# Performance work log

Hardware: AMD Instinct MI355X
Metric: run time of the kernel (lower is better)

## Reference

```python
import jax, jax.numpy as jnp
import numpy as np

H = 12           # num_heads
D_MODEL = 768
SCALE = (D_MODEL // H) ** -0.5  # qk_scale default: head_dim**-0.5


def _attn_mask(q, k, v, mask):
    # sim: (b, i, j); mask broadcast over query dim (mask.unsqueeze(1) in torch)
    sim = jnp.einsum('bid,bjd->bij', q, k) + mask[:, None, :]
    a = jax.nn.softmax(sim, axis=-1)
    return jnp.einsum('bij,bjd->bid', a, v)


def setup_inputs() -> dict:
    key = jax.random.key(0)
    k0, k1, k2, k3 = jax.random.split(key, 4)
    B, F, n, D = 16, 8, 196, 768
    N = 1 + F * n  # cls + frames*patches = 1569
    x = jax.random.normal(k0, (B, N, D), jnp.float32)
    x_mask = jax.random.normal(k1, (B, N), jnp.float32)  # additive attention mask
    Wqkv = jax.random.normal(k2, (3 * D, D), jnp.float32) * (D ** -0.5)
    Wproj = jax.random.normal(k3, (D, D), jnp.float32) * (D ** -0.5)
    bproj = jnp.zeros((D,), jnp.float32)
    return {"x": x, "x_mask": x_mask, "Wqkv": Wqkv, "Wproj": Wproj,
            "bproj": bproj, "f": F}


def reference(x, x_mask, Wqkv, Wproj, bproj, f):
    B, N, D = x.shape
    h = H
    d = D // h
    # qkv projection (qkv_bias=False), split into q,k,v
    qkv = x @ Wqkv.T                       # (B, N, 3D)
    q, k, v = jnp.split(qkv, 3, axis=-1)

    def to_heads(t):  # 'b n (h d) -> (b h) n d'
        return t.reshape(B, N, h, d).transpose(0, 2, 1, 3).reshape(B * h, N, d)

    q, k, v = map(to_heads, (q, k, v))
    mask = jnp.repeat(x_mask, h, axis=0)   # repeat_interleave over heads: (B*h, N)

    q = q * SCALE
    cls_q, q_ = q[:, :1], q[:, 1:]
    cls_k, k_ = k[:, :1], k[:, 1:]
    cls_v, v_ = v[:, :1], v[:, 1:]
    cls_mask, mask_ = mask[:, :1], mask[:, 1:]

    # cls token attends to everything
    cls_out = _attn_mask(cls_q, k, v, mask)            # (B*h, 1, d)

    # spatial attention: 'b (f n) d -> (b f) n d'
    n = (N - 1) // f
    q_ = q_.reshape(B * h * f, n, d)
    k_ = k_.reshape(B * h * f, n, d)
    v_ = v_.reshape(B * h * f, n, d)
    mask_ = mask_.reshape(B * h * f, n)

    # prepend cls k/v/mask to every frame group (r = f)
    cls_k = jnp.repeat(cls_k, f, axis=0)               # (B*h*f, 1, d)
    cls_v = jnp.repeat(cls_v, f, axis=0)
    cls_m = jnp.repeat(cls_mask, f, axis=0)            # (B*h*f, 1)
    k_ = jnp.concatenate([cls_k, k_], axis=1)          # (B*h*f, n+1, d)
    v_ = jnp.concatenate([cls_v, v_], axis=1)
    m2 = jnp.concatenate([cls_m, mask_], axis=1)       # (B*h*f, n+1)

    out = _attn_mask(q_, k_, v_, m2)                   # (B*h*f, n, d)
    out = out.reshape(B * h, f * n, d)                 # '(b f) n d -> b (f n) d'
    out = jnp.concatenate([cls_out, out], axis=1)      # (B*h, N, d)
    out = out.reshape(B, h, N, d).transpose(0, 2, 1, 3).reshape(B, N, D)
    return out @ Wproj.T + bproj
```

## Files before the change

kernel.cpp:

```cpp
#include <hip/hip_runtime.h>
#include <hip/hip_bf16.h>
#include <stdint.h>

#define Hh 12
#define Dm 768
#define Bb 16
#define Nt 1569
#define Ff 8
#define NC 196
#define BH 192
#define Mr 25104
#define CPW 224
#define VTW (8*CPW)
#define PLD 232
#define CLD 132

typedef __attribute__((ext_vector_type(8))) short bf16x8;
typedef __attribute__((ext_vector_type(4))) float f32x4;

typedef const __attribute__((address_space(1))) uint32_t guint;
typedef __attribute__((address_space(3))) uint32_t luint;

static __device__ __forceinline__ float bf2f(unsigned short u) {
  union { unsigned int i; float f; } v; v.i = ((unsigned int)u) << 16; return v.f;
}
static __device__ __forceinline__ unsigned short f2bf(float f) {
  __hip_bfloat16 h = __float2bfloat16(f);
  return __builtin_bit_cast(unsigned short, h);
}

__global__ void cast3_k(const float4* __restrict__ s0, ushort4* __restrict__ d0, int n0,
                        const float4* __restrict__ s1, ushort4* __restrict__ d1, int n1,
                        const float4* __restrict__ s2, ushort4* __restrict__ d2, int n2) {
  int nTot = n0 + n1 + n2;
  for (int i = blockIdx.x * blockDim.x + threadIdx.x; i < nTot; i += gridDim.x * blockDim.x) {
    const float4* s; ushort4* d; int off;
    if (i < n0) { s = s0; d = d0; off = i; }
    else if (i < n0 + n1) { s = s1; d = d1; off = i - n0; }
    else { s = s2; d = d2; off = i - n0 - n1; }
    float4 f = s[off];
    ushort4 u;
    u.x = f2bf(f.x); u.y = f2bf(f.y); u.z = f2bf(f.z); u.w = f2bf(f.w);
    d[off] = u;
  }
}

template<int MODE>
__global__ __launch_bounds__(256) void gemm_k(
    const __hip_bfloat16* __restrict__ A,
    const __hip_bfloat16* __restrict__ W,
    int M, int K,
    __hip_bfloat16* __restrict__ qh, __hip_bfloat16* __restrict__ kh,
    __hip_bfloat16* __restrict__ vT, __hip_bfloat16* __restrict__ vcls,
    const float* __restrict__ bias, float* __restrict__ outp)
{
  __shared__ __align__(16) unsigned short shmem[128 * CLD];
  unsigned short* ls0 = shmem;
  unsigned short* ls1 = shmem + 4096;
  unsigned short* ls2 = shmem + 8192;
  unsigned short* ls3 = shmem + 12288;

  const int tid = threadIdx.x;
  const int lane = tid & 63, wid = tid >> 6;
  const int waveM = wid >> 1, waveN = wid & 1;

  const int gridN = gridDim.x;
  const int nwg = gridDim.x * gridDim.y;
  int bid = blockIdx.y * gridN + blockIdx.x;
  int q8 = nwg >> 3, r8 = nwg & 7;
  int xcd = bid & 7, lid = bid >> 3;
  int swz = (xcd < r8 ? xcd * (q8 + 1) : r8 * (q8 + 1) + (xcd - r8) * q8) + lid;
  const int mBase = (swz / gridN) * 128, nBase = (swz % gridN) * 128;

  const int l15 = lane & 15, lg = lane >> 4;
  f32x4 acc[4][4] = {};
  const int nkt = K >> 6;
  for (int kt = 0; kt < nkt; ++kt) {
#pragma unroll
    for (int s = 0; s < 2; ++s) {
      int seg = s * 256 + tid;
      int row = seg >> 2, ks = seg & 3;
      int arow = mBase + row; if (arow >= M) arow = M - 1;
      int brow = nBase + row;
      const __hip_bfloat16* ap = A + (size_t)arow * K + kt * 64 + ks * 8;
      const __hip_bfloat16* wp = W + (size_t)brow * K + kt * 64 + ks * 8;
      __builtin_amdgcn_global_load_lds((guint*)ap,        (luint*)&ls0[seg * 8], 16, 0, 0);
      __builtin_amdgcn_global_load_lds((guint*)wp,        (luint*)&ls1[seg * 8], 16, 0, 0);
      __builtin_amdgcn_global_load_lds((guint*)(ap + 32), (luint*)&ls2[seg * 8], 16, 0, 0);
      __builtin_amdgcn_global_load_lds((guint*)(wp + 32), (luint*)&ls3[seg * 8], 16, 0, 0);
    }
    __syncthreads();
    bf16x8 aF[4], bF[4], aG[4], bG[4];
#pragma unroll
    for (int i = 0; i < 4; ++i) {
      int ro = (waveM * 64 + i * 16 + l15) * 32 + lg * 8;
      int co = (waveN * 64 + i * 16 + l15) * 32 + lg * 8;
      aF[i] = *reinterpret_cast<const bf16x8*>(&ls0[ro]);
      bF[i] = *reinterpret_cast<const bf16x8*>(&ls1[co]);
      aG[i] = *reinterpret_cast<const bf16x8*>(&ls2[ro]);
      bG[i] = *reinterpret_cast<const bf16x8*>(&ls3[co]);
    }
#pragma unroll
    for (int mi = 0; mi < 4; ++mi)
#pragma unroll
      for (int ni = 0; ni < 4; ++ni) {
        acc[mi][ni] = __builtin_amdgcn_mfma_f32_16x16x32_bf16(aF[mi], bF[ni], acc[mi][ni], 0, 0, 0);
        acc[mi][ni] = __builtin_amdgcn_mfma_f32_16x16x32_bf16(aG[mi], bG[ni], acc[mi][ni], 0, 0, 0);
      }
    __syncthreads();
  }

  if (MODE == 1) {
    const bool fullM = (mBase + 128 <= M);
#pragma unroll
    for (int mi = 0; mi < 4; ++mi)
#pragma unroll
      for (int ni = 0; ni < 4; ++ni)
#pragma unroll
        for (int r = 0; r < 4; ++r) {
          int grow = mBase + waveM * 64 + mi * 16 + lg * 4 + r;
          if (!fullM && grow >= M) continue;
          int gcol = nBase + waveN * 64 + ni * 16 + l15;
          outp[(size_t)grow * Dm + gcol] = acc[mi][ni][r] + bias[gcol];
        }
    return;
  }

  const int which = nBase / Dm;
  const int headBase = (nBase - which * Dm) >> 6;
  const float scl = (which == 0) ? 0.125f : 1.f;
  const bool fullM = (mBase + 128 <= M);

  if (fullM) {
    if (which < 2) {
#pragma unroll
      for (int mi = 0; mi < 4; ++mi)
#pragma unroll
        for (int ni = 0; ni < 4; ++ni)
#pragma unroll
          for (int r = 0; r < 4; ++r)
            shmem[(waveM * 64 + mi * 16 + lg * 4 + r) * CLD + (waveN * 64 + ni * 16 + l15)]
                = f2bf(acc[mi][ni][r] * scl);
      __syncthreads();
      __hip_bfloat16* dst = (which == 0) ? qh : kh;
      int row = tid >> 1, h = tid & 1;
      int grow = mBase + row;
      int b = grow / Nt, i = grow - b * Nt;
      const uint2* sp = reinterpret_cast<const uint2*>(&shmem[row * CLD + h * 64]);
      uint2* dp = reinterpret_cast<uint2*>(
          dst + ((size_t)(b * Hh + headBase + h) * Nt + i) * 64);
#pragma unroll
      for (int j = 0; j < 16; ++j) dp[j] = sp[j];
    } else {
#pragma unroll
      for (int mi = 0; mi < 4; ++mi)
#pragma unroll
        for (int ni = 0; ni < 4; ++ni)
#pragma unroll
          for (int r = 0; r < 4; ++r)
            shmem[(waveN * 64 + ni * 16 + l15) * CLD + (waveM * 64 + mi * 16 + lg * 4 + r)]
                = f2bf(acc[mi][ni][r]);
      __syncthreads();
      int lc = tid & 127, rhalf = tid >> 7;
      int h = lc >> 6, dc = lc & 63;
      int head = headBase + h;
#pragma unroll
      for (int g = 0; g < 8; ++g) {
        int row0 = rhalf * 64 + g * 8;
        int grow0 = mBase + row0;
        int b = grow0 / Nt, i0 = grow0 - b * Nt;
        const unsigned short* sp = &shmem[lc * CLD + row0];
        if (i0 >= 1 && i0 + 8 <= Nt) {
          int j0 = i0 - 1, cc = j0 / NC, key = j0 - cc * NC;
          if (key + 8 <= NC) {
            int bh = b * Hh + head;
            __hip_bfloat16* p = vT + ((size_t)bh * 64 + dc) * VTW + cc * CPW + key;
            if ((key & 1) == 0) {
              const unsigned int* s4 = reinterpret_cast<const unsigned int*>(sp);
              unsigned int* d4 = reinterpret_cast<unsigned int*>(p);
              d4[0] = s4[0]; d4[1] = s4[1]; d4[2] = s4[2]; d4[3] = s4[3];
            } else {
#pragma unroll
              for (int j = 0; j < 8; ++j)
                p[j] = __builtin_bit_cast(__hip_bfloat16, sp[j]);
            }
            continue;
          }
        }
#pragma unroll
        for (int j = 0; j < 8; ++j) {
          int grow = grow0 + j;
          int bb = grow / Nt, ii = grow - bb * Nt;
          int bh2 = bb * Hh + head;
          unsigned short val = sp[j];
          if (ii == 0) {
            vcls[bh2 * 64 + dc] = __builtin_bit_cast(__hip_bfloat16, val);
          } else {
            int jj = ii - 1, cc2 = jj / NC, k2 = jj - cc2 * NC;
            vT[((size_t)bh2 * 64 + dc) * VTW + cc2 * CPW + k2]
                = __builtin_bit_cast(__hip_bfloat16, val);
          }
        }
      }
    }
  } else {
#pragma unroll
    for (int mi = 0; mi < 4; ++mi)
#pragma unroll
      for (int ni = 0; ni < 4; ++ni)
#pragma unroll
        for (int r = 0; r < 4; ++r) {
          int grow = mBase + waveM * 64 + mi * 16 + lg * 4 + r;
          if (grow >= M) continue;
          int gcol = nBase + waveN * 64 + ni * 16 + l15;
          float v = acc[mi][ni][r];
          int b = grow / Nt, i = grow - b * Nt;
          int hcol = gcol - which * Dm;
          int head = hcol >> 6, dc = hcol & 63;
          int bh = b * Hh + head;
          if (which == 0) {
            qh[((size_t)bh * Nt + i) * 64 + dc] = __float2bfloat16(v * 0.125f);
          } else if (which == 1) {
            kh[((size_t)bh * Nt + i) * 64 + dc] = __float2bfloat16(v);
          } else {
            if (i == 0) vcls[bh * 64 + dc] = __float2bfloat16(v);
            else {
              int j = i - 1; int cc = j / NC, key = j - cc * NC;
              vT[((size_t)bh * 64 + dc) * VTW + cc * CPW + key] = __float2bfloat16(v);
            }
          }
        }
  }
}

__global__ __launch_bounds__(256) void cls_attn_k(
    const __hip_bfloat16* __restrict__ qh, const __hip_bfloat16* __restrict__ kh,
    const __hip_bfloat16* __restrict__ vT, const __hip_bfloat16* __restrict__ vcls,
    const float* __restrict__ x_mask, __hip_bfloat16* __restrict__ ao)
{
  const int bh = blockIdx.x, b = bh / Hh, head = bh - b * Hh;
  const int tid = threadIdx.x;
  __shared__ float sS[Nt];
  __shared__ float qv[64];
  __shared__ float red[256];
  if (tid < 64) qv[tid] = __bfloat162float(qh[((size_t)bh * Nt) * 64 + tid]);
  __syncthreads();
  float lmax = -1e30f;
  for (int j = tid; j < Nt; j += 256) {
    const __hip_bfloat16* kr = kh + ((size_t)bh * Nt + j) * 64;
    float dot = 0.f;
#pragma unroll
    for (int d0 = 0; d0 < 64; d0 += 8) {
      bf16x8 kv = *reinterpret_cast<const bf16x8*>(kr + d0);
#pragma unroll
      for (int i = 0; i < 8; ++i) dot += qv[d0 + i] * bf2f((unsigned short)kv[i]);
    }
    float s = dot + x_mask[b * Nt + j];
    sS[j] = s;
    lmax = fmaxf(lmax, s);
  }
  red[tid] = lmax; __syncthreads();
  for (int off = 128; off > 0; off >>= 1) {
    if (tid < off) red[tid] = fmaxf(red[tid], red[tid + off]);
    __syncthreads();
  }
  float m = red[0]; __syncthreads();
  float lsum = 0.f;
  for (int j = tid; j < Nt; j += 256) { float e = __expf(sS[j] - m); sS[j] = e; lsum += e; }
  red[tid] = lsum; __syncthreads();
  for (int off = 128; off > 0; off >>= 1) {
    if (tid < off) red[tid] += red[tid + off];
    __syncthreads();
  }
  float rden = 1.f / red[0]; __syncthreads();
  int dc = tid & 63, part = tid >> 6;
  float partial = 0.f;
  if (part == 0) partial = sS[0] * __bfloat162float(vcls[bh * 64 + dc]);
  const __hip_bfloat16* vrow = vT + ((size_t)bh * 64 + dc) * VTW;
  for (int cc = part * 2; cc < part * 2 + 2; ++cc) {
    int base = 1 + cc * NC;
    const __hip_bfloat16* vc2 = vrow + cc * CPW;
    int key = 0;
    for (; key + 8 <= NC; key += 8) {
      bf16x8 vv = *reinterpret_cast<const bf16x8*>(vc2 + key);
#pragma unroll
      for (int i = 0; i < 8; ++i)
        partial += sS[base + key + i] * bf2f((unsigned short)vv[i]);
    }
    for (; key < NC; ++key)
      partial += sS[base + key] * __bfloat162float(vc2[key]);
  }
  red[tid] = partial; __syncthreads();
  if (tid < 64) {
    float o = (red[tid] + red[tid + 64] + red[tid + 128] + red[tid + 192]) * rden;
    ao[((size_t)b * Nt) * Dm + head * 64 + dc] = __float2bfloat16(o);
  }
}

__global__ __launch_bounds__(64, 4) void chunk_attn_k(
    const __hip_bfloat16* __restrict__ qh, const __hip_bfloat16* __restrict__ kh,
    const __hip_bfloat16* __restrict__ vT, const __hip_bfloat16* __restrict__ vcls,
    const float* __restrict__ x_mask, __hip_bfloat16* __restrict__ ao)
{
  const int bid = blockIdx.x;
  const int work = (bid & 7) * 2496 + (bid >> 3);
  const int g = work / 13;
  const int rtile = work - g * 13;
  const int bh = g >> 3, c = g & 7;
  const int b = bh / Hh, head = bh - b * Hh;
  const int lane = threadIdx.x;
  const int l15 = lane & 15, lg = lane >> 4;
  __shared__ __align__(16) __hip_bfloat16 ldsP[16 * PLD];

  int qlrow = rtile * 16 + l15;
  int qtok = 1 + c * NC + qlrow; if (qtok > Nt - 1) qtok = Nt - 1;
  const __hip_bfloat16* qp = qh + ((size_t)bh * Nt + qtok) * 64;
  bf16x8 aQ0 = *reinterpret_cast<const bf16x8*>(qp + lg * 8);
  bf16x8 aQ1 = *reinterpret_cast<const bf16x8*>(qp + 32 + lg * 8);

  float pc0;
  {
    const __hip_bfloat16* kc = kh + (size_t)bh * Nt * 64;
    bf16x8 ck0 = *reinterpret_cast<const bf16x8*>(kc + lg * 8);
    bf16x8 ck1 = *reinterpret_cast<const bf16x8*>(kc + 32 + lg * 8);
    float p = 0.f;
#pragma unroll
    for (int i = 0; i < 8; ++i)
      p += bf2f((unsigned short)aQ0[i]) * bf2f((unsigned short)ck0[i])
         + bf2f((unsigned short)aQ1[i]) * bf2f((unsigned short)ck1[i]);
    p += __shfl_xor(p, 16);
    p += __shfl_xor(p, 32);
    pc0 = p + x_mask[b * Nt];
  }

  const int kbase = 1 + c * NC;
  f32x4 S[13];
  bf16x8 kb0[13], kb1[13];
  float mv[13];
#define LD(i) { int key = (i) * 16 + l15; int kt2 = kbase + key; if (kt2 > Nt - 1) kt2 = Nt - 1; \
    const __hip_bfloat16* kp = kh + ((size_t)bh * Nt + kt2) * 64; \
    kb0[i] = *reinterpret_cast<const bf16x8*>(kp + lg * 8); \
    kb1[i] = *reinterpret_cast<const bf16x8*>(kp + 32 + lg * 8); \
    mv[i] = (key < NC) ? x_mask[b * Nt + kbase + key] : -1e30f; }
#define MM(i) { f32x4 sa = {}; \
    sa = __builtin_amdgcn_mfma_f32_16x16x32_bf16(aQ0, kb0[i], sa, 0, 0, 0); \
    sa = __builtin_amdgcn_mfma_f32_16x16x32_bf16(aQ1, kb1[i], sa, 0, 0, 0); \
    S[i][0] = sa[0] + mv[i]; S[i][1] = sa[1] + mv[i]; \
    S[i][2] = sa[2] + mv[i]; S[i][3] = sa[3] + mv[i]; }
  LD(0) LD(1) LD(2)
  __builtin_amdgcn_sched_barrier(0);
  LD(3) LD(4) LD(5)  MM(0) MM(1) MM(2)
  __builtin_amdgcn_sched_barrier(0);
  LD(6) LD(7) LD(8)  MM(3) MM(4) MM(5)
  __builtin_amdgcn_sched_barrier(0);
  LD(9) LD(10) LD(11)  MM(6) MM(7) MM(8)
  __builtin_amdgcn_sched_barrier(0);
  LD(12)  MM(9) MM(10) MM(11)
  MM(12)
#undef LD
#undef MM

  float pcls[4], rden[4];
#pragma unroll
  for (int r = 0; r < 4; ++r) {
    float m = -1e30f;
#pragma unroll
    for (int nt = 0; nt < 13; ++nt) m = fmaxf(m, S[nt][r]);
    m = fmaxf(m, __shfl_xor(m, 1));
    m = fmaxf(m, __shfl_xor(m, 2));
    m = fmaxf(m, __shfl_xor(m, 4));
    m = fmaxf(m, __shfl_xor(m, 8));
    float sc = __shfl(pc0, lg * 4 + r);
    m = fmaxf(m, sc);
    float sum = 0.f;
#pragma unroll
    for (int nt = 0; nt < 13; ++nt) { float e = __expf(S[nt][r] - m); S[nt][r] = e; sum += e; }
    sum += __shfl_xor(sum, 1);
    sum += __shfl_xor(sum, 2);
    sum += __shfl_xor(sum, 4);
    sum += __shfl_xor(sum, 8);
    float pc = __expf(sc - m);
    pcls[r] = pc;
    rden[r] = 1.f / (sum + pc);
  }

#pragma unroll
  for (int nt = 0; nt < 13; ++nt)
#pragma unroll
    for (int r = 0; r < 4; ++r)
      ldsP[(lg * 4 + r) * PLD + nt * 16 + l15] = __float2bfloat16(S[nt][r]);
#pragma unroll
  for (int r = 0; r < 4; ++r)
    ldsP[l15 * PLD + 208 + lg * 4 + r] = __float2bfloat16(0.f);
  __syncthreads();

  f32x4 O[4] = {};
#define PVK(kt) { \
    bf16x8 aP = *reinterpret_cast<const bf16x8*>(&ldsP[l15 * PLD + (kt) * 32 + lg * 8]); \
    { bf16x8 bV = *reinterpret_cast<const bf16x8*>(vT + ((size_t)bh * 64 + (0 * 16 + l15)) * VTW + c * CPW + (kt) * 32 + lg * 8); \
      O[0] = __builtin_amdgcn_mfma_f32_16x16x32_bf16(aP, bV, O[0], 0, 0, 0); } \
    { bf16x8 bV = *reinterpret_cast<const bf16x8*>(vT + ((size_t)bh * 64 + (1 * 16 + l15)) * VTW + c * CPW + (kt) * 32 + lg * 8); \
      O[1] = __builtin_amdgcn_mfma_f32_16x16x32_bf16(aP, bV, O[1], 0, 0, 0); } \
    { bf16x8 bV = *reinterpret_cast<const bf16x8*>(vT + ((size_t)bh * 64 + (2 * 16 + l15)) * VTW + c * CPW + (kt) * 32 + lg * 8); \
      O[2] = __builtin_amdgcn_mfma_f32_16x16x32_bf16(aP, bV, O[2], 0, 0, 0); } \
    { bf16x8 bV = *reinterpret_cast<const bf16x8*>(vT + ((size_t)bh * 64 + (3 * 16 + l15)) * VTW + c * CPW + (kt) * 32 + lg * 8); \
      O[3] = __builtin_amdgcn_mfma_f32_16x16x32_bf16(aP, bV, O[3], 0, 0, 0); } }
  PVK(0) PVK(1)
  __builtin_amdgcn_sched_barrier(0);
  PVK(2) PVK(3)
  __builtin_amdgcn_sched_barrier(0);
  PVK(4) PVK(5)
  __builtin_amdgcn_sched_barrier(0);
  PVK(6)
#undef PVK

#pragma unroll
  for (int ni = 0; ni < 4; ++ni) {
    int dc = ni * 16 + l15;
    float vc = __bfloat162float(vcls[bh * 64 + dc]);
#pragma unroll
    for (int r = 0; r < 4; ++r) {
      int lrow = rtile * 16 + lg * 4 + r;
      if (lrow < NC) {
        float o = (O[ni][r] + pcls[r] * vc) * rden[r];
        int tok = 1 + c * NC + lrow;
        ao[((size_t)b * Nt + tok) * Dm + head * 64 + dc] = __float2bfloat16(o);
      }
    }
  }
}

extern "C" void kernel_launch(void* const* d_in, const int* in_sizes, int n_in,
                              void* d_out, int out_size, void* d_ws, size_t ws_size,
                              hipStream_t stream) {
  const float* x     = (const float*)d_in[0];
  const float* xmask = (const float*)d_in[1];
  const float* wqkv  = (const float*)d_in[2];
  const float* wproj = (const float*)d_in[3];
  const float* bproj = (const float*)d_in[4];
  float* outp = (float*)d_out;

  char* ws = (char*)d_ws;
  size_t off = 0;
  auto alloc = [&](size_t bytes) {
    char* p = ws + off;
    off += (bytes + 255) & ~(size_t)255;
    return p;
  };
  __hip_bfloat16* xb     = (__hip_bfloat16*)alloc((size_t)Mr * Dm * 2);
  __hip_bfloat16* wqkvb  = (__hip_bfloat16*)alloc((size_t)3 * Dm * Dm * 2);
  __hip_bfloat16* wprojb = (__hip_bfloat16*)alloc((size_t)Dm * Dm * 2);
  __hip_bfloat16* qh     = (__hip_bfloat16*)alloc((size_t)BH * Nt * 64 * 2);
  __hip_bfloat16* kh     = (__hip_bfloat16*)alloc((size_t)BH * Nt * 64 * 2);
  __hip_bfloat16* vT     = (__hip_bfloat16*)alloc((size_t)BH * 64 * VTW * 2);
  __hip_bfloat16* vcls   = (__hip_bfloat16*)alloc((size_t)BH * 64 * 2);
  __hip_bfloat16* ao = xb;

  cast3_k<<<2048, 256, 0, stream>>>((const float4*)x, (ushort4*)xb, Mr * Dm / 4,
                                    (const float4*)wqkv, (ushort4*)wqkvb, 3 * Dm * Dm / 4,
                                    (const float4*)wproj, (ushort4*)wprojb, Dm * Dm / 4);

  gemm_k<0><<<dim3(18, 197), 256, 0, stream>>>(xb, wqkvb, Mr, Dm, qh, kh, vT, vcls, nullptr, nullptr);

  cls_attn_k<<<BH, 256, 0, stream>>>(qh, kh, vT, vcls, xmask, ao);
  chunk_attn_k<<<13 * BH * Ff, 64, 0, stream>>>(qh, kh, vT, vcls, xmask, ao);

  gemm_k<1><<<dim3(6, 197), 256, 0, stream>>>(ao, wprojb, Mr, Dm, nullptr, nullptr, nullptr, nullptr, bproj, outp);
}
```

Before: 367.0 us.

## Enlarge GEMM tiles to 256x256 with double-buffered swizzled LDS pipeline

The GEMM kernel moves from 128x128 tiles with 4 waves to 256x256 tiles with 8 waves (512 threads). It double-buffers the global-to-LDS loads, so the next K-slab prefetches while MFMAs run on the current one, and uses explicit waitcnt and barriers. It also XOR-swizzles the LDS layout to avoid bank conflicts. This targets load latency and synchronisation stalls in the QKV and projection GEMMs, but adds register and LDS pressure (about 130KB of shared memory) and only about 300 workgroups for the projection GEMM.

```diff
diff --git a/kernel.cpp b/kernel.cpp
--- a/kernel.cpp
+++ b/kernel.cpp
@@ -13,7 +13,7 @@
 #define CPW 224
 #define VTW (8*CPW)
 #define PLD 232
-#define CLD 132
+#define CLD2 260
 
 typedef __attribute__((ext_vector_type(8))) short bf16x8;
 typedef __attribute__((ext_vector_type(4))) float f32x4;
@@ -46,7 +46,7 @@
 }
 
 template<int MODE>
-__global__ __launch_bounds__(256) void gemm_k(
+__global__ __launch_bounds__(512, 2) void gemm_k(
     const __hip_bfloat16* __restrict__ A,
     const __hip_bfloat16* __restrict__ W,
     int M, int K,
@@ -54,15 +54,12 @@
     __hip_bfloat16* __restrict__ vT, __hip_bfloat16* __restrict__ vcls,
     const float* __restrict__ bias, float* __restrict__ outp)
 {
-  __shared__ __align__(16) unsigned short shmem[128 * CLD];
-  unsigned short* ls0 = shmem;
-  unsigned short* ls1 = shmem + 4096;
-  unsigned short* ls2 = shmem + 8192;
-  unsigned short* ls3 = shmem + 12288;
+  __shared__ __align__(16) unsigned short shmem[66560];
 
   const int tid = threadIdx.x;
   const int lane = tid & 63, wid = tid >> 6;
-  const int waveM = wid >> 1, waveN = wid & 1;
+  const int wm = wid >> 2, wn = wid & 3;
+  const int l15 = lane & 15, lg = lane >> 4;
 
   const int gridN = gridDim.x;
   const int nwg = gridDim.x * gridDim.y;
@@ -70,57 +67,85 @@
   int q8 = nwg >> 3, r8 = nwg & 7;
   int xcd = bid & 7, lid = bid >> 3;
   int swz = (xcd < r8 ? xcd * (q8 + 1) : r8 * (q8 + 1) + (xcd - r8) * q8) + lid;
-  const int mBase = (swz / gridN) * 128, nBase = (swz % gridN) * 128;
-
-  const int l15 = lane & 15, lg = lane >> 4;
-  f32x4 acc[4][4] = {};
-  const int nkt = K >> 6;
-  for (int kt = 0; kt < nkt; ++kt) {
-#pragma unroll
-    for (int s = 0; s < 2; ++s) {
-      int seg = s * 256 + tid;
-      int row = seg >> 2, ks = seg & 3;
+  const int mBase = (swz / gridN) * 256, nBase = (swz % gridN) * 256;
+
+  auto STAGE = [&](int d, int kt) {
+    unsigned short* la = shmem + d * 32768;
+    unsigned short* lb = la + 16384;
+#pragma unroll
+    for (int c2 = 0; c2 < 4; ++c2) {
+      int idx = c2 * 512 + tid;
+      int row = idx >> 3;
+      int kob = ((idx & 7) * 16) ^ (idx & 0x60);
       int arow = mBase + row; if (arow >= M) arow = M - 1;
       int brow = nBase + row;
-      const __hip_bfloat16* ap = A + (size_t)arow * K + kt * 64 + ks * 8;
-      const __hip_bfloat16* wp = W + (size_t)brow * K + kt * 64 + ks * 8;
-      __builtin_amdgcn_global_load_lds((guint*)ap,        (luint*)&ls0[seg * 8], 16, 0, 0);
-      __builtin_amdgcn_global_load_lds((guint*)wp,        (luint*)&ls1[seg * 8], 16, 0, 0);
-      __builtin_amdgcn_global_load_lds((guint*)(ap + 32), (luint*)&ls2[seg * 8], 16, 0, 0);
-      __builtin_amdgcn_global_load_lds((guint*)(wp + 32), (luint*)&ls3[seg * 8], 16, 0, 0);
-    }
-    __syncthreads();
-    bf16x8 aF[4], bF[4], aG[4], bG[4];
-#pragma unroll
-    for (int i = 0; i < 4; ++i) {
-      int ro = (waveM * 64 + i * 16 + l15) * 32 + lg * 8;
-      int co = (waveN * 64 + i * 16 + l15) * 32 + lg * 8;
-      aF[i] = *reinterpret_cast<const bf16x8*>(&ls0[ro]);
-      bF[i] = *reinterpret_cast<const bf16x8*>(&ls1[co]);
-      aG[i] = *reinterpret_cast<const bf16x8*>(&ls2[ro]);
-      bG[i] = *reinterpret_cast<const bf16x8*>(&ls3[co]);
-    }
-#pragma unroll
-    for (int mi = 0; mi < 4; ++mi)
-#pragma unroll
-      for (int ni = 0; ni < 4; ++ni) {
-        acc[mi][ni] = __builtin_amdgcn_mfma_f32_16x16x32_bf16(aF[mi], bF[ni], acc[mi][ni], 0, 0, 0);
-        acc[mi][ni] = __builtin_amdgcn_mfma_f32_16x16x32_bf16(aG[mi], bG[ni], acc[mi][ni], 0, 0, 0);
+      __builtin_amdgcn_global_load_lds(
+          (guint*)((const char*)(A + (size_t)arow * K + kt * 64) + kob),
+          (luint*)&la[idx * 8], 16, 0, 0);
+      __builtin_amdgcn_global_load_lds(
+          (guint*)((const char*)(W + (size_t)brow * K + kt * 64) + kob),
+          (luint*)&lb[idx * 8], 16, 0, 0);
+    }
+  };
+
+  f32x4 acc[8][4] = {};
+  const int nkt = K >> 6;
+
+  STAGE(0, 0);
+  STAGE(1, 1);
+  asm volatile("s_waitcnt vmcnt(8)" ::: "memory");
+  __builtin_amdgcn_s_barrier();
+  __builtin_amdgcn_sched_barrier(0);
+
+#pragma unroll 1
+  for (int kt = 0; kt < nkt; ++kt) {
+    const int d = kt & 1;
+    const char* la = (const char*)(shmem + d * 32768);
+    const char* lb = la + 32768;
+#pragma unroll
+    for (int ks = 0; ks < 2; ++ks) {
+      bf16x8 aF[8], bF[4];
+#pragma unroll
+      for (int i = 0; i < 8; ++i) {
+        int row = wm * 128 + i * 16 + l15;
+        int ko = (ks * 64 + lg * 16) ^ ((row << 3) & 0x60);
+        aF[i] = *reinterpret_cast<const bf16x8*>(la + row * 128 + ko);
       }
-    __syncthreads();
+#pragma unroll
+      for (int i = 0; i < 4; ++i) {
+        int row = wn * 64 + i * 16 + l15;
+        int ko = (ks * 64 + lg * 16) ^ ((row << 3) & 0x60);
+        bF[i] = *reinterpret_cast<const bf16x8*>(lb + row * 128 + ko);
+      }
+#pragma unroll
+      for (int mi = 0; mi < 8; ++mi)
+#pragma unroll
+        for (int ni = 0; ni < 4; ++ni)
+          acc[mi][ni] = __builtin_amdgcn_mfma_f32_16x16x32_bf16(aF[mi], bF[ni], acc[mi][ni], 0, 0, 0);
+    }
+    __builtin_amdgcn_sched_barrier(0);
+    __builtin_amdgcn_s_barrier();
+    if (kt + 2 < nkt) {
+      STAGE(d, kt + 2);
+      asm volatile("s_waitcnt vmcnt(8)" ::: "memory");
+    } else {
+      asm volatile("s_waitcnt vmcnt(0)" ::: "memory");
+    }
+    __builtin_amdgcn_s_barrier();
+    __builtin_amdgcn_sched_barrier(0);
   }
 
   if (MODE == 1) {
-    const bool fullM = (mBase + 128 <= M);
-#pragma unroll
-    for (int mi = 0; mi < 4; ++mi)
+    const bool fullM = (mBase + 256 <= M);
+#pragma unroll
+    for (int mi = 0; mi < 8; ++mi)
 #pragma unroll
       for (int ni = 0; ni < 4; ++ni)
 #pragma unroll
         for (int r = 0; r < 4; ++r) {
-          int grow = mBase + waveM * 64 + mi * 16 + lg * 4 + r;
+          int grow = mBase + wm * 128 + mi * 16 + lg * 4 + r;
           if (!fullM && grow >= M) continue;
-          int gcol = nBase + waveN * 64 + ni * 16 + l15;
+          int gcol = nBase + wn * 64 + ni * 16 + l15;
           outp[(size_t)grow * Dm + gcol] = acc[mi][ni][r] + bias[gcol];
         }
     return;
@@ -129,47 +154,50 @@
   const int which = nBase / Dm;
   const int headBase = (nBase - which * Dm) >> 6;
   const float scl = (which == 0) ? 0.125f : 1.f;
-  const bool fullM = (mBase + 128 <= M);
+  const bool fullM = (mBase + 256 <= M);
 
   if (fullM) {
     if (which < 2) {
 #pragma unroll
-      for (int mi = 0; mi < 4; ++mi)
+      for (int mi = 0; mi < 8; ++mi)
 #pragma unroll
         for (int ni = 0; ni < 4; ++ni)
 #pragma unroll
           for (int r = 0; r < 4; ++r)
-            shmem[(waveM * 64 + mi * 16 + lg * 4 + r) * CLD + (waveN * 64 + ni * 16 + l15)]
+            shmem[(wm * 128 + mi * 16 + lg * 4 + r) * CLD2 + (wn * 64 + ni * 16 + l15)]
                 = f2bf(acc[mi][ni][r] * scl);
       __syncthreads();
       __hip_bfloat16* dst = (which == 0) ? qh : kh;
-      int row = tid >> 1, h = tid & 1;
+      int row = tid >> 1, hpart = tid & 1;
       int grow = mBase + row;
       int b = grow / Nt, i = grow - b * Nt;
-      const uint2* sp = reinterpret_cast<const uint2*>(&shmem[row * CLD + h * 64]);
-      uint2* dp = reinterpret_cast<uint2*>(
-          dst + ((size_t)(b * Hh + headBase + h) * Nt + i) * 64);
-#pragma unroll
-      for (int j = 0; j < 16; ++j) dp[j] = sp[j];
+#pragma unroll
+      for (int hh = 0; hh < 2; ++hh) {
+        int hsel = hpart * 2 + hh;
+        const uint2* sp = reinterpret_cast<const uint2*>(&shmem[row * CLD2 + hsel * 64]);
+        uint2* dp = reinterpret_cast<uint2*>(
+            dst + ((size_t)(b * Hh + headBase + hsel) * Nt + i) * 64);
+#pragma unroll
+        for (int j = 0; j < 16; ++j) dp[j] = sp[j];
+      }
     } else {
 #pragma unroll
-      for (int mi = 0; mi < 4; ++mi)
+      for (int mi = 0; mi < 8; ++mi)
 #pragma unroll
         for (int ni = 0; ni < 4; ++ni)
 #pragma unroll
           for (int r = 0; r < 4; ++r)
-            shmem[(waveN * 64 + ni * 16 + l15) * CLD + (waveM * 64 + mi * 16 + lg * 4 + r)]
+            shmem[(wn * 64 + ni * 16 + l15) * CLD2 + (wm * 128 + mi * 16 + lg * 4 + r)]
                 = f2bf(acc[mi][ni][r]);
       __syncthreads();
-      int lc = tid & 127, rhalf = tid >> 7;
-      int h = lc >> 6, dc = lc & 63;
-      int head = headBase + h;
-#pragma unroll
-      for (int g = 0; g < 8; ++g) {
-        int row0 = rhalf * 64 + g * 8;
+      int lc = tid & 255, rblk = tid >> 8;
+      int head = headBase + (lc >> 6), dc = lc & 63;
+#pragma unroll
+      for (int gi = 0; gi < 16; ++gi) {
+        int row0 = rblk * 128 + gi * 8;
         int grow0 = mBase + row0;
         int b = grow0 / Nt, i0 = grow0 - b * Nt;
-        const unsigned short* sp = &shmem[lc * CLD + row0];
+        const unsigned short* sp = &shmem[lc * CLD2 + row0];
         if (i0 >= 1 && i0 + 8 <= Nt) {
           int j0 = i0 - 1, cc = j0 / NC, key = j0 - cc * NC;
           if (key + 8 <= NC) {
@@ -205,14 +233,14 @@
     }
   } else {
 #pragma unroll
-    for (int mi = 0; mi < 4; ++mi)
+    for (int mi = 0; mi < 8; ++mi)
 #pragma unroll
       for (int ni = 0; ni < 4; ++ni)
 #pragma unroll
         for (int r = 0; r < 4; ++r) {
-          int grow = mBase + waveM * 64 + mi * 16 + lg * 4 + r;
+          int grow = mBase + wm * 128 + mi * 16 + lg * 4 + r;
           if (grow >= M) continue;
-          int gcol = nBase + waveN * 64 + ni * 16 + l15;
+          int gcol = nBase + wn * 64 + ni * 16 + l15;
           float v = acc[mi][ni][r];
           int b = grow / Nt, i = grow - b * Nt;
           int hcol = gcol - which * Dm;
@@ -460,10 +488,10 @@
                                     (const float4*)wqkv, (ushort4*)wqkvb, 3 * Dm * Dm / 4,
                                     (const float4*)wproj, (ushort4*)wprojb, Dm * Dm / 4);
 
-  gemm_k<0><<<dim3(18, 197), 256, 0, stream>>>(xb, wqkvb, Mr, Dm, qh, kh, vT, vcls, nullptr, nullptr);
+  gemm_k<0><<<dim3(9, 99), 512, 0, stream>>>(xb, wqkvb, Mr, Dm, qh, kh, vT, vcls, nullptr, nullptr);
 
   cls_attn_k<<<BH, 256, 0, stream>>>(qh, kh, vT, vcls, xmask, ao);
   chunk_attn_k<<<13 * BH * Ff, 64, 0, stream>>>(qh, kh, vT, vcls, xmask, ao);
 
-  gemm_k<1><<<dim3(6, 197), 256, 0, stream>>>(ao, wprojb, Mr, Dm, nullptr, nullptr, nullptr, nullptr, bproj, outp);
-}
+  gemm_k<1><<<dim3(3, 99), 512, 0, stream>>>(ao, wprojb, Mr, Dm, nullptr, nullptr, nullptr, nullptr, bproj, outp);
+}
```

Measured after the change: 406.0 us. 1.11x slower.
